# Performance work log

Hardware: AMD Instinct MI355X
Metric: run time of the kernel (lower is better)

The kernel has to match this reference:

```python
import jax, jax.numpy as jnp
import numpy as np
from jax import lax

HEADS = 4
SR = 4
LN_EPS = 1e-5


def setup_inputs() -> dict:
    key = jax.random.key(0)
    ks = jax.random.split(key, 8)
    B, N, C = 8, 4096, 256
    w_scale = 0.05  # keep attention logits in a sane range
    return {
        "x": jax.random.normal(ks[0], (B, N, C), jnp.float32),
        "h": 64,
        "w": 64,
        "Wq": jax.random.normal(ks[1], (C, C), jnp.float32) * w_scale,
        "Wkv": jax.random.normal(ks[2], (C, 2 * C), jnp.float32) * w_scale,
        "sr_w": jax.random.normal(ks[3], (C, C, SR, SR), jnp.float32) * w_scale,
        "sr_b": jnp.zeros((C,), jnp.float32),
        "ln_g": jnp.ones((C,), jnp.float32),
        "ln_b": jnp.zeros((C,), jnp.float32),
        "Wo": jax.random.normal(ks[4], (C, C), jnp.float32) * w_scale,
        "bo": jnp.zeros((C,), jnp.float32),
    }


def _layernorm(x, g, b):
    mu = x.mean(-1, keepdims=True)
    var = ((x - mu) ** 2).mean(-1, keepdims=True)
    return (x - mu) * lax.rsqrt(var + LN_EPS) * g + b


def reference(x, h, w, Wq, Wkv, sr_w, sr_b, ln_g, ln_b, Wo, bo):
    B, N, C = x.shape
    hd = C // HEADS
    scale = hd ** -0.5
    # Q projection -> [B, H, N, hd]
    q = (x @ Wq).reshape(B, N, HEADS, hd).transpose(0, 2, 1, 3)
    # spatial reduction of K/V tokens: strided conv + LayerNorm
    x_kv = x.transpose(0, 2, 1).reshape(B, C, h, w)  # b (h w) c -> b c h w
    x_kv = lax.conv_general_dilated(
        x_kv, sr_w, window_strides=(SR, SR), padding="VALID",
        dimension_numbers=("NCHW", "OIHW", "NCHW"))
    x_kv = x_kv + sr_b[None, :, None, None]
    Nk = (h // SR) * (w // SR)
    x_kv = x_kv.reshape(B, C, Nk).transpose(0, 2, 1)  # b c h w -> b (h w) c
    x_kv = _layernorm(x_kv, ln_g, ln_b)
    # KV projection -> k, v each [B, H, Nk, hd]
    kv = (x_kv @ Wkv).reshape(B, Nk, 2, HEADS, hd)
    k = kv[:, :, 0].transpose(0, 2, 1, 3)
    v = kv[:, :, 1].transpose(0, 2, 1, 3)
    # attention: full [B, H, N, Nk] score matrix, softmax over kv axis
    att = jax.nn.softmax(jnp.einsum("bhxd,bhyd->bhxy", q, k) * scale, axis=-1)
    out = jnp.einsum("bhxy,bhyd->bhxd", att, v)
    out = out.transpose(0, 2, 1, 3).reshape(B, N, C)  # b h l d -> b l (h d)
    return out @ Wo + bo
```

## Files before the change

kernel.cpp:

```cpp
#include <hip/hip_runtime.h>

typedef __bf16 bf16;
typedef bf16 bf16x8 __attribute__((ext_vector_type(8)));
typedef bf16 bf16x4 __attribute__((ext_vector_type(4)));
typedef float f32x4 __attribute__((ext_vector_type(4)));

#define MFMA16(a, b, c) __builtin_amdgcn_mfma_f32_16x16x32_bf16(a, b, c, 0, 0, 0)

__device__ __forceinline__ void gload_lds16(const bf16* g, bf16* l) {
  __builtin_amdgcn_global_load_lds(
      (const __attribute__((address_space(1))) void*)g,
      (__attribute__((address_space(3))) void*)l, 16, 0, 0);
}

__global__ void k_prep(const float* __restrict__ x, const float* __restrict__ Wq,
                       const float* __restrict__ Wkv, const float* __restrict__ Wo,
                       const float* __restrict__ srw,
                       bf16* __restrict__ x_bf, bf16* __restrict__ WqT,
                       bf16* __restrict__ WkvT, bf16* __restrict__ WoT,
                       bf16* __restrict__ srwT) {
  int bid = blockIdx.x, tid = threadIdx.x;
  if (bid < 8192) {
    int i = (bid * 256 + tid) * 4;
    float4 v = *(const float4*)(x + i);
    bf16x4 o;
    o[0] = (bf16)v.x; o[1] = (bf16)v.y; o[2] = (bf16)v.z; o[3] = (bf16)v.w;
    *(bf16x4*)(x_bf + i) = o;
  } else if (bid < 9216) {
    int id = (bid - 8192) * 256 + tid;
    if (id < 65536) {
      int c = id >> 8, r = id & 255;
      WqT[id] = (bf16)Wq[r * 256 + c];
    } else if (id < 196608) {
      int l = id - 65536;
      int c = l >> 8, r = l & 255;
      WkvT[l] = (bf16)Wkv[r * 512 + c];
    } else {
      int l = id - 196608;
      int c = l >> 8, r = l & 255;
      WoT[l] = (bf16)Wo[r * 256 + c];
    }
  } else {
    int id4 = ((bid - 9216) * 256 + tid) * 4;
    int o = id4 >> 12, rem = id4 & 4095;
    int i = rem >> 4, p = rem & 15;
    float4 v = *(const float4*)(srw + id4);
    srwT[(o << 12) + ((p + 0) << 8) + i] = (bf16)v.x;
    srwT[(o << 12) + ((p + 1) << 8) + i] = (bf16)v.y;
    srwT[(o << 12) + ((p + 2) << 8) + i] = (bf16)v.z;
    srwT[(o << 12) + ((p + 3) << 8) + i] = (bf16)v.w;
  }
}

template <int AMODE, int EMODE>
__global__ __launch_bounds__(256, 2) void k_gemm(
    const bf16* __restrict__ A, const bf16* __restrict__ Bt,
    void* __restrict__ Cout, const float* __restrict__ bias,
    int M, int N, int K) {
  constexpr int LDT = 72;
  __shared__ alignas(16) bf16 As[64 * LDT];
  __shared__ alignas(16) bf16 Bs[64 * LDT];
  int tid = threadIdx.x;
  int m0 = blockIdx.x * 64, n0 = blockIdx.y * 64;
  int kbeg = blockIdx.z * K;
  int wave = tid >> 6, lane = tid & 63;
  int quad = lane >> 4, l16 = lane & 15;

  f32x4 acc[4];
#pragma unroll
  for (int i = 0; i < 4; i++) acc[i] = (f32x4){0.f, 0.f, 0.f, 0.f};

  for (int k0 = kbeg; k0 < kbeg + K; k0 += 64) {
#pragma unroll
    for (int t = 0; t < 2; t++) {
      int c = tid + t * 256;
      int row = c >> 3, c8 = (c & 7) * 8;
      *(bf16x8*)&As[row * LDT + c8] =
          *(const bf16x8*)(A + (size_t)(m0 + row) * K + k0 + c8);
      *(bf16x8*)&Bs[row * LDT + c8] =
          *(const bf16x8*)(Bt + (size_t)(n0 + row) * K + k0 + c8);
    }
    __syncthreads();
#pragma unroll
    for (int kk = 0; kk < 64; kk += 32) {
      bf16x8 af = *(const bf16x8*)&As[(wave * 16 + l16) * LDT + kk + quad * 8];
#pragma unroll
      for (int nt = 0; nt < 4; nt++) {
        bf16x8 bfr = *(const bf16x8*)&Bs[(nt * 16 + l16) * LDT + kk + quad * 8];
        acc[nt] = MFMA16(af, bfr, acc[nt]);
      }
    }
    __syncthreads();
  }

  int rbase = m0 + wave * 16 + quad * 4;
#pragma unroll
  for (int nt = 0; nt < 4; nt++) {
    int col = n0 + nt * 16 + l16;
#pragma unroll
    for (int r = 0; r < 4; r++) {
      float v = acc[nt][r];
      int row = rbase + r;
      if constexpr (EMODE == 2) {
        int b = row >> 8, key = row & 255;
        int isv = col >> 8, c2 = col & 255;
        int hh = c2 >> 6, d = c2 & 63;
        int bh = b * 4 + hh;
        bf16* dst = (bf16*)Cout;
        if (isv == 0)
          dst[(((size_t)bh) * 256 + key) * 64 + (d ^ ((key & 7) << 3))] = (bf16)v;
        else
          dst[32 * 256 * 64 + (((size_t)bh) * 64 + d) * 256 + (key ^ ((d & 7) << 3))] = (bf16)v;
      } else {
        ((float*)Cout)[(size_t)row * N + col] = v + bias[col];
      }
    }
  }
}

template <int AMODE, int EMODE>
__global__ __launch_bounds__(256, 2) void k_gemm128(
    const bf16* __restrict__ A, const bf16* __restrict__ Bt,
    void* __restrict__ Cout, const float* __restrict__ bias,
    int M, int N, int K) {
  __shared__ alignas(16) bf16 As[128 * 64];
  __shared__ alignas(16) bf16 Bs[128 * 64];
  int tid = threadIdx.x;
  int m0 = blockIdx.x * 128, n0 = blockIdx.y * 128;
  int kbeg = blockIdx.z * K;
  int wave = tid >> 6, lane = tid & 63;
  int quad = lane >> 4, l16 = lane & 15;
  int wr = wave >> 1, wc = wave & 1;

  f32x4 acc[4][4];
#pragma unroll
  for (int i = 0; i < 4; i++)
#pragma unroll
    for (int j = 0; j < 4; j++) acc[i][j] = (f32x4){0.f, 0.f, 0.f, 0.f};

  for (int k0 = kbeg; k0 < kbeg + K; k0 += 64) {
#pragma unroll
    for (int t = 0; t < 4; t++) {
      int chunk = wave * 4 + t;
      int row = chunk * 8 + (lane >> 3);
      int c8 = (lane & 7) * 8;
      const bf16* asrc;
      if constexpr (AMODE == 0) {
        asrc = A + (size_t)(m0 + row) * K + k0 + c8;
      } else {
        int m = m0 + row;
        int b = m >> 8, tt = m & 255;
        int oh = tt >> 4, ow = tt & 15;
        int p = k0 >> 8;
        int kh = p >> 2, kw = p & 3;
        int tok = (oh * 4 + kh) * 64 + ow * 4 + kw;
        asrc = A + ((size_t)(b * 4096 + tok) << 8) + (k0 & 255) + c8;
      }
      gload_lds16(asrc, As + chunk * 512);
      gload_lds16(Bt + (size_t)(n0 + row) * ((AMODE == 1) ? 4096 : K) + k0 + c8,
                  Bs + chunk * 512);
    }
    __syncthreads();
#pragma unroll
    for (int kk = 0; kk < 64; kk += 32) {
      bf16x8 af[4], bfr[4];
#pragma unroll
      for (int mt = 0; mt < 4; mt++)
        af[mt] = *(const bf16x8*)&As[(wr * 64 + mt * 16 + l16) * 64 + kk + quad * 8];
#pragma unroll
      for (int nt = 0; nt < 4; nt++)
        bfr[nt] = *(const bf16x8*)&Bs[(wc * 64 + nt * 16 + l16) * 64 + kk + quad * 8];
#pragma unroll
      for (int mt = 0; mt < 4; mt++)
#pragma unroll
        for (int nt = 0; nt < 4; nt++)
          acc[mt][nt] = MFMA16(af[mt], bfr[nt], acc[mt][nt]);
    }
    __syncthreads();
  }

#pragma unroll
  for (int mt = 0; mt < 4; mt++) {
    int rbase = m0 + wr * 64 + mt * 16 + quad * 4;
#pragma unroll
    for (int nt = 0; nt < 4; nt++) {
      int col = n0 + wc * 64 + nt * 16 + l16;
#pragma unroll
      for (int r = 0; r < 4; r++) {
        float v = acc[mt][nt][r];
        int row = rbase + r;
        if constexpr (EMODE == 3) {
          ((float*)Cout)[(size_t)row * N + col] = v + bias[col];
        } else if constexpr (EMODE == 5) {
          int b2 = row >> 12, tok = row & 4095;
          int hh = col >> 6, d = col & 63;
          ((bf16*)Cout)[(((size_t)(b2 * 4 + hh)) * 4096 + tok) * 64 + d] = (bf16)v;
        } else {
          ((float*)Cout)[((size_t)blockIdx.z * M + row) * N + col] = v;
        }
      }
    }
  }
}

__global__ void k_ln(const float* __restrict__ part, const float* __restrict__ srb,
                     const float* __restrict__ g, const float* __restrict__ bb,
                     bf16* __restrict__ out) {
  int row = blockIdx.x * 4 + (threadIdx.x >> 6);
  int lane = threadIdx.x & 63;
  size_t off = (size_t)row * 256 + lane * 4;
  float4 v = *(const float4*)&part[off];
#pragma unroll
  for (int z = 1; z < 8; z++) {
    float4 p = *(const float4*)&part[(size_t)z * 2048 * 256 + off];
    v.x += p.x; v.y += p.y; v.z += p.z; v.w += p.w;
  }
  int c = lane * 4;
  v.x += srb[c + 0]; v.y += srb[c + 1]; v.z += srb[c + 2]; v.w += srb[c + 3];
  float s = v.x + v.y + v.z + v.w;
#pragma unroll
  for (int i = 1; i < 64; i <<= 1) s += __shfl_xor(s, i, 64);
  float mu = s * (1.f / 256.f);
  float d0 = v.x - mu, d1 = v.y - mu, d2 = v.z - mu, d3 = v.w - mu;
  float q = d0 * d0 + d1 * d1 + d2 * d2 + d3 * d3;
#pragma unroll
  for (int i = 1; i < 64; i <<= 1) q += __shfl_xor(q, i, 64);
  float rs = rsqrtf(q * (1.f / 256.f) + 1e-5f);
  bf16x4 o;
  o[0] = (bf16)(d0 * rs * g[c + 0] + bb[c + 0]);
  o[1] = (bf16)(d1 * rs * g[c + 1] + bb[c + 1]);
  o[2] = (bf16)(d2 * rs * g[c + 2] + bb[c + 2]);
  o[3] = (bf16)(d3 * rs * g[c + 3] + bb[c + 3]);
  *(bf16x4*)&out[(size_t)row * 256 + c] = o;
}

__global__ __launch_bounds__(256, 3) void k_attn(
    const bf16* __restrict__ Qg,
    const bf16* __restrict__ Kg,
    const bf16* __restrict__ Vg,
    bf16* __restrict__ O) {
  int bh = blockIdx.x, qt = blockIdx.y;
  int b = bh >> 2, h = bh & 3;
  int tid = threadIdx.x, wave = tid >> 6, lane = tid & 63;
  int quad = lane >> 4, l16 = lane & 15;

  __shared__ alignas(16) bf16 smem[24576];
  bf16* Ks = smem;
  bf16* Vs = smem + 16384;

  const bf16* Kbh = Kg + ((size_t)bh << 14);
  const bf16* Vbh = Vg + ((size_t)bh << 14);

#pragma unroll
  for (int t = 0; t < 8; t++) {
    int chunk = t * 4 + wave;
    gload_lds16(Kbh + chunk * 512 + lane * 8, Ks + chunk * 512);
  }
#pragma unroll
  for (int t = 0; t < 4; t++) {
    int chunk = t * 4 + wave;
    gload_lds16(Vbh + (chunk * 4 + (lane >> 4)) * 256 + (lane & 15) * 8,
                Vs + chunk * 512);
  }

  const bf16* qrow =
      Qg + (((size_t)bh * 4096) + qt * 64 + wave * 16 + l16) * 64 + quad * 8;
  bf16x8 aq0 = *(const bf16x8*)(qrow);
  bf16x8 aq1 = *(const bf16x8*)(qrow + 32);

  __syncthreads();

  f32x4 s[16];
#pragma unroll
  for (int i = 0; i < 16; i++) s[i] = (f32x4){0.f, 0.f, 0.f, 0.f};
#pragma unroll
  for (int nt = 0; nt < 16; nt++) {
    int krow = nt * 16 + l16;
    const bf16* kb = Ks + krow * 64;
    int sw = (krow & 7) << 3;
    bf16x8 b0 = *(const bf16x8*)(kb + ((quad * 8) ^ sw));
    bf16x8 b1 = *(const bf16x8*)(kb + ((32 + quad * 8) ^ sw));
    s[nt] = MFMA16(aq0, b0, s[nt]);
    s[nt] = MFMA16(aq1, b1, s[nt]);
  }

  const float scale = 0.125f;
#pragma unroll
  for (int r = 0; r < 4; r++) {
    float m = -1e30f;
#pragma unroll
    for (int nt = 0; nt < 16; nt++) m = fmaxf(m, s[nt][r]);
#pragma unroll
    for (int i = 1; i < 16; i <<= 1) m = fmaxf(m, __shfl_xor(m, i, 64));
    float sum = 0.f;
#pragma unroll
    for (int nt = 0; nt < 16; nt++) {
      float e = __expf((s[nt][r] - m) * scale);
      s[nt][r] = e;
      sum += e;
    }
#pragma unroll
    for (int i = 1; i < 16; i <<= 1) sum += __shfl_xor(sum, i, 64);
    float inv = 1.f / sum;
#pragma unroll
    for (int nt = 0; nt < 16; nt++) s[nt][r] *= inv;
  }

  __syncthreads();

#pragma unroll
  for (int nt = 0; nt < 16; nt++)
#pragma unroll
    for (int r = 0; r < 4; r++) {
      int prow = wave * 16 + quad * 4 + r;
      Ks[prow * 256 + ((nt * 16 + l16) ^ ((prow & 7) << 3))] = (bf16)s[nt][r];
    }

  int arow = wave * 16 + l16;
  int asw = (arow & 7) << 3;
  const bf16* pb = Ks + arow * 256;
  f32x4 o[4];
#pragma unroll
  for (int i = 0; i < 4; i++) o[i] = (f32x4){0.f, 0.f, 0.f, 0.f};
#pragma unroll
  for (int k0 = 0; k0 < 128; k0 += 32) {
    bf16x8 ap = *(const bf16x8*)(pb + ((k0 + quad * 8) ^ asw));
#pragma unroll
    for (int nt = 0; nt < 4; nt++) {
      int vrow = nt * 16 + l16;
      bf16x8 bv = *(const bf16x8*)(Vs + vrow * 128 + ((k0 + quad * 8) ^ ((vrow & 7) << 3)));
      o[nt] = MFMA16(ap, bv, o[nt]);
    }
  }

  __syncthreads();
#pragma unroll
  for (int t = 0; t < 4; t++) {
    int chunk = t * 4 + wave;
    gload_lds16(Vbh + (chunk * 4 + (lane >> 4)) * 256 + 128 + (lane & 15) * 8,
                Vs + chunk * 512);
  }
  __syncthreads();

#pragma unroll
  for (int k0 = 128; k0 < 256; k0 += 32) {
    bf16x8 ap = *(const bf16x8*)(pb + ((k0 + quad * 8) ^ asw));
    int kl = k0 - 128;
#pragma unroll
    for (int nt = 0; nt < 4; nt++) {
      int vrow = nt * 16 + l16;
      bf16x8 bv = *(const bf16x8*)(Vs + vrow * 128 + ((kl + quad * 8) ^ ((vrow & 7) << 3)));
      o[nt] = MFMA16(ap, bv, o[nt]);
    }
  }

  size_t orow = (size_t)b * 4096 + qt * 64 + wave * 16 + quad * 4;
#pragma unroll
  for (int nt = 0; nt < 4; nt++) {
    int col = h * 64 + nt * 16 + l16;
#pragma unroll
    for (int r = 0; r < 4; r++) O[(orow + r) * 256 + col] = (bf16)o[nt][r];
  }
}

extern "C" void kernel_launch(void* const* d_in, const int* in_sizes, int n_in,
                              void* d_out, int out_size, void* d_ws, size_t ws_size,
                              hipStream_t stream) {
  (void)in_sizes; (void)n_in; (void)out_size; (void)ws_size;
  const float* x   = (const float*)d_in[0];
  const float* Wq  = (const float*)d_in[3];
  const float* Wkv = (const float*)d_in[4];
  const float* srw = (const float*)d_in[5];
  const float* srb = (const float*)d_in[6];
  const float* lng = (const float*)d_in[7];
  const float* lnb = (const float*)d_in[8];
  const float* Wo  = (const float*)d_in[9];
  const float* bo  = (const float*)d_in[10];
  float* out = (float*)d_out;

  char* ws = (char*)d_ws;
  bf16*  x_bf  = (bf16*)(ws + 0);
  bf16*  AObuf = (bf16*)(ws + 16777216);
  float* convp = (float*)(ws + 33554432);
  bf16*  qbuf  = (bf16*)(ws + 33554432);
  bf16*  WqT   = (bf16*)(ws + 50331648);
  bf16*  WkvT  = (bf16*)(ws + 50462720);
  bf16*  WoT   = (bf16*)(ws + 50724864);
  bf16*  srwT  = (bf16*)(ws + 50855936);
  bf16*  xln   = (bf16*)(ws + 52953088);
  bf16*  kvbuf = (bf16*)(ws + 54001664);

  k_prep<<<10240, 256, 0, stream>>>(x, Wq, Wkv, Wo, srw, x_bf, WqT, WkvT, WoT, srwT);
  k_gemm128<1, 4><<<dim3(16, 2, 8), 256, 0, stream>>>(x_bf, srwT, convp, nullptr, 2048, 256, 512);
  k_ln<<<512, 256, 0, stream>>>(convp, srb, lng, lnb, xln);
  k_gemm<0, 2><<<dim3(32, 8), 256, 0, stream>>>(xln, WkvT, kvbuf, nullptr, 2048, 512, 256);
  k_gemm128<0, 5><<<dim3(256, 2), 256, 0, stream>>>(x_bf, WqT, qbuf, nullptr, 32768, 256, 256);
  k_attn<<<dim3(32, 64), 256, 0, stream>>>(qbuf, kvbuf, kvbuf + (size_t)32 * 256 * 64, AObuf);
  k_gemm128<0, 3><<<dim3(256, 2), 256, 0, stream>>>(AObuf, WoT, out, bo, 32768, 256, 256);
}
```

Before: 181.7 us.

## Fuse Q projection into attention kernel and pipeline V in quarter chunks

Removes the separate Q-projection GEMM and its bf16 Q buffer. Each attention block now computes its 64x64 Q tile from x_bf and a per-head slice of a swizzled WqT staged in LDS. V is streamed through two 64-column double buffers, and K is loaded into LDS after the Q compute. This saves one launch plus the write and re-read of Q. In exchange every attention block reloads a 256x64 weight slice and re-reads the x rows, once for each of the 4 heads, and the LDS choreography gains extra barriers.

```diff
diff --git a/kernel.cpp b/kernel.cpp
--- a/kernel.cpp
+++ b/kernel.cpp
@@ -30,7 +30,7 @@
     int id = (bid - 8192) * 256 + tid;
     if (id < 65536) {
       int c = id >> 8, r = id & 255;
-      WqT[id] = (bf16)Wq[r * 256 + c];
+      WqT[c * 256 + (r ^ ((c & 7) << 3))] = (bf16)Wq[r * 256 + c];
     } else if (id < 196608) {
       int l = id - 65536;
       int c = l >> 8, r = l & 255;
@@ -191,10 +191,6 @@
         int row = rbase + r;
         if constexpr (EMODE == 3) {
           ((float*)Cout)[(size_t)row * N + col] = v + bias[col];
-        } else if constexpr (EMODE == 5) {
-          int b2 = row >> 12, tok = row & 4095;
-          int hh = col >> 6, d = col & 63;
-          ((bf16*)Cout)[(((size_t)(b2 * 4 + hh)) * 4096 + tok) * 64 + d] = (bf16)v;
         } else {
           ((float*)Cout)[((size_t)blockIdx.z * M + row) * N + col] = v;
         }
@@ -235,7 +231,8 @@
 }
 
 __global__ __launch_bounds__(256, 3) void k_attn(
-    const bf16* __restrict__ Qg,
+    const bf16* __restrict__ xbf,
+    const bf16* __restrict__ WqT,
     const bf16* __restrict__ Kg,
     const bf16* __restrict__ Vg,
     bf16* __restrict__ O) {
@@ -245,30 +242,73 @@
   int quad = lane >> 4, l16 = lane & 15;
 
   __shared__ alignas(16) bf16 smem[24576];
-  bf16* Ks = smem;
-  bf16* Vs = smem + 16384;
+  bf16* R0  = smem;
+  bf16* R2a = smem + 16384;
+  bf16* R2b = smem + 20480;
 
   const bf16* Kbh = Kg + ((size_t)bh << 14);
   const bf16* Vbh = Vg + ((size_t)bh << 14);
+  const bf16* Wqh = WqT + ((size_t)(h * 64) << 8);
 
 #pragma unroll
   for (int t = 0; t < 8; t++) {
     int chunk = t * 4 + wave;
-    gload_lds16(Kbh + chunk * 512 + lane * 8, Ks + chunk * 512);
-  }
-#pragma unroll
-  for (int t = 0; t < 4; t++) {
+    gload_lds16(Wqh + chunk * 512 + lane * 8, R0 + chunk * 512);
+  }
+#pragma unroll
+  for (int t = 0; t < 2; t++) {
+    int chunk = wave * 2 + t;
+    gload_lds16(Vbh + (chunk * 8 + (lane >> 3)) * 256 + 0 + (lane & 7) * 8,
+                R2a + chunk * 512);
+  }
+  const bf16* xrow =
+      xbf + (((size_t)(b * 4096 + qt * 64 + wave * 16 + l16)) << 8) + quad * 8;
+  bf16x8 ax[8];
+#pragma unroll
+  for (int j = 0; j < 8; j++) ax[j] = *(const bf16x8*)(xrow + j * 32);
+
+  __syncthreads();
+
+  f32x4 q[4];
+#pragma unroll
+  for (int i = 0; i < 4; i++) q[i] = (f32x4){0.f, 0.f, 0.f, 0.f};
+#pragma unroll
+  for (int j = 0; j < 8; j++) {
+#pragma unroll
+    for (int nt = 0; nt < 4; nt++) {
+      int wrow = nt * 16 + l16;
+      bf16x8 bw = *(const bf16x8*)&R0[wrow * 256 +
+                                      ((j * 32 + quad * 8) ^ ((wrow & 7) << 3))];
+      q[nt] = MFMA16(ax[j], bw, q[nt]);
+    }
+  }
+  __syncthreads();
+
+#pragma unroll
+  for (int nt = 0; nt < 4; nt++)
+#pragma unroll
+    for (int r = 0; r < 4; r++) {
+      int qr = wave * 16 + quad * 4 + r;
+      R2b[qr * 64 + ((nt * 16 + l16) ^ ((qr & 7) << 3))] = (bf16)q[nt][r];
+    }
+#pragma unroll
+  for (int t = 0; t < 8; t++) {
     int chunk = t * 4 + wave;
-    gload_lds16(Vbh + (chunk * 4 + (lane >> 4)) * 256 + (lane & 15) * 8,
-                Vs + chunk * 512);
-  }
-
-  const bf16* qrow =
-      Qg + (((size_t)bh * 4096) + qt * 64 + wave * 16 + l16) * 64 + quad * 8;
-  bf16x8 aq0 = *(const bf16x8*)(qrow);
-  bf16x8 aq1 = *(const bf16x8*)(qrow + 32);
-
+    gload_lds16(Kbh + chunk * 512 + lane * 8, R0 + chunk * 512);
+  }
   __syncthreads();
+
+  int arow = wave * 16 + l16;
+  int asw = (arow & 7) << 3;
+  bf16x8 aq0 = *(const bf16x8*)&R2b[arow * 64 + ((quad * 8) ^ asw)];
+  bf16x8 aq1 = *(const bf16x8*)&R2b[arow * 64 + ((32 + quad * 8) ^ asw)];
+  asm volatile("s_waitcnt lgkmcnt(0)" ::: "memory");
+#pragma unroll
+  for (int t = 0; t < 2; t++) {
+    int chunk = wave * 2 + t;
+    gload_lds16(Vbh + (chunk * 8 + (lane >> 3)) * 256 + 64 + (lane & 7) * 8,
+                R2b + chunk * 512);
+  }
 
   f32x4 s[16];
 #pragma unroll
@@ -276,7 +316,7 @@
 #pragma unroll
   for (int nt = 0; nt < 16; nt++) {
     int krow = nt * 16 + l16;
-    const bf16* kb = Ks + krow * 64;
+    const bf16* kb = R0 + krow * 64;
     int sw = (krow & 7) << 3;
     bf16x8 b0 = *(const bf16x8*)(kb + ((quad * 8) ^ sw));
     bf16x8 b1 = *(const bf16x8*)(kb + ((32 + quad * 8) ^ sw));
@@ -313,44 +353,40 @@
 #pragma unroll
     for (int r = 0; r < 4; r++) {
       int prow = wave * 16 + quad * 4 + r;
-      Ks[prow * 256 + ((nt * 16 + l16) ^ ((prow & 7) << 3))] = (bf16)s[nt][r];
-    }
-
-  int arow = wave * 16 + l16;
-  int asw = (arow & 7) << 3;
-  const bf16* pb = Ks + arow * 256;
+      R0[prow * 256 + ((nt * 16 + l16) ^ ((prow & 7) << 3))] = (bf16)s[nt][r];
+    }
+
+  const bf16* pb = R0 + arow * 256;
   f32x4 o[4];
 #pragma unroll
   for (int i = 0; i < 4; i++) o[i] = (f32x4){0.f, 0.f, 0.f, 0.f};
-#pragma unroll
-  for (int k0 = 0; k0 < 128; k0 += 32) {
-    bf16x8 ap = *(const bf16x8*)(pb + ((k0 + quad * 8) ^ asw));
-#pragma unroll
-    for (int nt = 0; nt < 4; nt++) {
-      int vrow = nt * 16 + l16;
-      bf16x8 bv = *(const bf16x8*)(Vs + vrow * 128 + ((k0 + quad * 8) ^ ((vrow & 7) << 3)));
-      o[nt] = MFMA16(ap, bv, o[nt]);
-    }
-  }
-
-  __syncthreads();
-#pragma unroll
-  for (int t = 0; t < 4; t++) {
-    int chunk = t * 4 + wave;
-    gload_lds16(Vbh + (chunk * 4 + (lane >> 4)) * 256 + 128 + (lane & 15) * 8,
-                Vs + chunk * 512);
-  }
-  __syncthreads();
-
-#pragma unroll
-  for (int k0 = 128; k0 < 256; k0 += 32) {
-    bf16x8 ap = *(const bf16x8*)(pb + ((k0 + quad * 8) ^ asw));
-    int kl = k0 - 128;
-#pragma unroll
-    for (int nt = 0; nt < 4; nt++) {
-      int vrow = nt * 16 + l16;
-      bf16x8 bv = *(const bf16x8*)(Vs + vrow * 128 + ((kl + quad * 8) ^ ((vrow & 7) << 3)));
-      o[nt] = MFMA16(ap, bv, o[nt]);
+
+#pragma unroll
+  for (int cq = 0; cq < 4; cq++) {
+    const bf16* Vbuf = (cq & 1) ? R2b : R2a;
+#pragma unroll
+    for (int k0 = 0; k0 < 64; k0 += 32) {
+      bf16x8 ap = *(const bf16x8*)(pb + ((cq * 64 + k0 + quad * 8) ^ asw));
+#pragma unroll
+      for (int nt = 0; nt < 4; nt++) {
+        int vrow = nt * 16 + l16;
+        bf16x8 bv = *(const bf16x8*)&Vbuf[vrow * 64 +
+                                          ((k0 + quad * 8) ^ ((vrow & 7) << 3))];
+        o[nt] = MFMA16(ap, bv, o[nt]);
+      }
+    }
+    if (cq < 3) {
+      __syncthreads();
+      if (cq < 2) {
+        bf16* nb = (cq & 1) ? R2b : R2a;
+#pragma unroll
+        for (int t = 0; t < 2; t++) {
+          int chunk = wave * 2 + t;
+          gload_lds16(Vbh + (chunk * 8 + (lane >> 3)) * 256 + (cq + 2) * 64 +
+                          (lane & 7) * 8,
+                      nb + chunk * 512);
+        }
+      }
     }
   }
 
@@ -382,7 +418,6 @@
   bf16*  x_bf  = (bf16*)(ws + 0);
   bf16*  AObuf = (bf16*)(ws + 16777216);
   float* convp = (float*)(ws + 33554432);
-  bf16*  qbuf  = (bf16*)(ws + 33554432);
   bf16*  WqT   = (bf16*)(ws + 50331648);
   bf16*  WkvT  = (bf16*)(ws + 50462720);
   bf16*  WoT   = (bf16*)(ws + 50724864);
@@ -394,7 +429,6 @@
   k_gemm128<1, 4><<<dim3(16, 2, 8), 256, 0, stream>>>(x_bf, srwT, convp, nullptr, 2048, 256, 512);
   k_ln<<<512, 256, 0, stream>>>(convp, srb, lng, lnb, xln);
   k_gemm<0, 2><<<dim3(32, 8), 256, 0, stream>>>(xln, WkvT, kvbuf, nullptr, 2048, 512, 256);
-  k_gemm128<0, 5><<<dim3(256, 2), 256, 0, stream>>>(x_bf, WqT, qbuf, nullptr, 32768, 256, 256);
-  k_attn<<<dim3(32, 64), 256, 0, stream>>>(qbuf, kvbuf, kvbuf + (size_t)32 * 256 * 64, AObuf);
+  k_attn<<<dim3(32, 64), 256, 0, stream>>>(x_bf, WqT, kvbuf, kvbuf + (size_t)32 * 256 * 64, AObuf);
   k_gemm128<0, 3><<<dim3(256, 2), 256, 0, stream>>>(AObuf, WoT, out, bo, 32768, 256, 256);
 }
```

After: 177.0 us. 2.6% less time.
